# Optimization experiments

Measured on AMD Instinct MI355X. Metric: run time of the kernel, lower is better.

The kernel has to match this reference:

```python
import jax, jax.numpy as jnp
import numpy as np

ALPHA = 0.2      # LeakyReLU negative slope
NEG_BIG = -9e15  # mask value from the original module


def setup_inputs() -> dict:
    key = jax.random.key(0)
    kx, ka, kW, ka1, ka2, kb = jax.random.split(key, 6)
    B, N, F_in, F_out = 8, 2048, 256, 128
    x = jax.random.normal(kx, (B, N, F_in), dtype=jnp.float32)
    adj = (jax.random.uniform(ka, (B, N, N)) < 0.1).astype(jnp.float32)
    adj = adj.at[:, jnp.arange(N), jnp.arange(N)].set(1.0)
    # parameters (xavier-uniform-ish scaling)
    W = jax.random.normal(kW, (F_out, F_in), dtype=jnp.float32) * np.sqrt(2.0 / (F_in + F_out))
    a1 = jax.random.normal(ka1, (F_out,), dtype=jnp.float32) * np.sqrt(2.0 / (2 * F_out + 1))
    a2 = jax.random.normal(ka2, (F_out,), dtype=jnp.float32) * np.sqrt(2.0 / (2 * F_out + 1))
    a_b = jax.random.normal(kb, (1,), dtype=jnp.float32) * 0.01
    return {"x": x, "adj": adj, "W": W, "a1": a1, "a2": a2, "a_b": a_b}


def reference(x, adj, W, a1, a2, a_b):
    # h = W(input): [B, N, F_out]
    h = jnp.einsum('bnf,of->bno', x, W)
    # a([h_i, h_j]) == a1.h_i + a2.h_j + bias  (exact decomposition of the concat)
    s1 = h @ a1  # [B, N] contribution of row-repeated node i
    s2 = h @ a2  # [B, N] contribution of tiled node j
    e = jax.nn.leaky_relu(s1[:, :, None] + s2[:, None, :] + a_b[0], negative_slope=ALPHA)  # [B,N,N]
    att = jnp.where(adj > 0, e, NEG_BIG)
    att = jax.nn.softmax(att, axis=1)  # softmax over dim=1, as in the original
    # dropout is a no-op in eval mode
    att = att * adj
    h_prime = jnp.einsum('bij,bjo->bio', att, h)
    return jax.nn.elu(h_prime)  # concat=True -> ELU
```

## Files before the change

kernel.cpp:

```cpp
#include <hip/hip_runtime.h>
#include <stdint.h>

typedef unsigned int  uint32;
typedef unsigned long long u64;

#define L2E 1.44269504088896340736f

typedef float f32x4 __attribute__((ext_vector_type(4)));
typedef short bf16x8 __attribute__((ext_vector_type(8)));

__device__ __forceinline__ unsigned short f2bf(float f){
  uint32 u = __float_as_uint(f);
  u += 0x7fffu + ((u >> 16) & 1u);
  return (unsigned short)(u >> 16);
}


__global__ __launch_bounds__(256) void k_h(const float* __restrict__ x,
                                           const float* __restrict__ W,
                                           const float* __restrict__ a1,
                                           const float* __restrict__ a2,
                                           const float* __restrict__ ab,
                                           float* __restrict__ h,
                                           float* __restrict__ E1,
                                           float* __restrict__ E2p){
  __shared__ unsigned short xs[2][64][72];
  __shared__ unsigned short wsm[2][128][72];
  const int tid = threadIdx.x;
  const int wv = tid >> 6, lane = tid & 63;
  const int r = lane & 15, kg = lane >> 4;
  const int row0 = blockIdx.x * 64;

  f32x4 acc[8];
  #pragma unroll
  for (int of = 0; of < 8; ++of) acc[of] = (f32x4){0.f,0.f,0.f,0.f};

  for (int kc = 0; kc < 4; ++kc){
    if (kc) __syncthreads();
    #pragma unroll
    for (int it = 0; it < 4; ++it){
      int idx = tid + it * 256;
      int row = idx >> 4, f = (idx & 15) * 4;
      float4 v = *(const float4*)(x + (size_t)(row0 + row) * 256 + kc * 64 + f);
      ushort4 hi, lo;
      { unsigned short hh = f2bf(v.x); float rr = v.x - __uint_as_float(((uint32)hh)<<16); hi.x = hh; lo.x = f2bf(rr); }
      { unsigned short hh = f2bf(v.y); float rr = v.y - __uint_as_float(((uint32)hh)<<16); hi.y = hh; lo.y = f2bf(rr); }
      { unsigned short hh = f2bf(v.z); float rr = v.z - __uint_as_float(((uint32)hh)<<16); hi.z = hh; lo.z = f2bf(rr); }
      { unsigned short hh = f2bf(v.w); float rr = v.w - __uint_as_float(((uint32)hh)<<16); hi.w = hh; lo.w = f2bf(rr); }
      *(ushort4*)&xs[0][row][f] = hi;
      *(ushort4*)&xs[1][row][f] = lo;
    }
    #pragma unroll
    for (int it = 0; it < 8; ++it){
      int idx = tid + it * 256;
      int o = idx >> 4, f = (idx & 15) * 4;
      float4 v = *(const float4*)(W + (size_t)o * 256 + kc * 64 + f);
      ushort4 hi, lo;
      { unsigned short hh = f2bf(v.x); float rr = v.x - __uint_as_float(((uint32)hh)<<16); hi.x = hh; lo.x = f2bf(rr); }
      { unsigned short hh = f2bf(v.y); float rr = v.y - __uint_as_float(((uint32)hh)<<16); hi.y = hh; lo.y = f2bf(rr); }
      { unsigned short hh = f2bf(v.z); float rr = v.z - __uint_as_float(((uint32)hh)<<16); hi.z = hh; lo.z = f2bf(rr); }
      { unsigned short hh = f2bf(v.w); float rr = v.w - __uint_as_float(((uint32)hh)<<16); hi.w = hh; lo.w = f2bf(rr); }
      *(ushort4*)&wsm[0][o][f] = hi;
      *(ushort4*)&wsm[1][o][f] = lo;
    }
    __syncthreads();
    #pragma unroll
    for (int kk = 0; kk < 2; ++kk){
      bf16x8 ah = *(const bf16x8*)&xs[0][wv*16 + r][kk*32 + kg*8];
      bf16x8 al = *(const bf16x8*)&xs[1][wv*16 + r][kk*32 + kg*8];
      #pragma unroll
      for (int of = 0; of < 8; ++of){
        bf16x8 bh = *(const bf16x8*)&wsm[0][of*16 + r][kk*32 + kg*8];
        bf16x8 bl = *(const bf16x8*)&wsm[1][of*16 + r][kk*32 + kg*8];
        acc[of] = __builtin_amdgcn_mfma_f32_16x16x32_bf16(ah, bh, acc[of], 0, 0, 0);
        acc[of] = __builtin_amdgcn_mfma_f32_16x16x32_bf16(ah, bl, acc[of], 0, 0, 0);
        acc[of] = __builtin_amdgcn_mfma_f32_16x16x32_bf16(al, bh, acc[of], 0, 0, 0);
      }
    }
  }
  #pragma unroll
  for (int of = 0; of < 8; ++of)
    #pragma unroll
    for (int q = 0; q < 4; ++q)
      h[(size_t)(row0 + wv*16 + kg*4 + q) * 128 + of*16 + r] = acc[of][q];

  float p1[4] = {0,0,0,0}, p2[4] = {0,0,0,0};
  #pragma unroll
  for (int of = 0; of < 8; ++of){
    float w1 = a1[of*16 + r], w2 = a2[of*16 + r];
    #pragma unroll
    for (int q = 0; q < 4; ++q){
      p1[q] = fmaf(acc[of][q], w1, p1[q]);
      p2[q] = fmaf(acc[of][q], w2, p2[q]);
    }
  }
  #pragma unroll
  for (int off = 8; off; off >>= 1)
    #pragma unroll
    for (int q = 0; q < 4; ++q){
      p1[q] += __shfl_xor(p1[q], off);
      p2[q] += __shfl_xor(p2[q], off);
    }
  if (r == 0){
    float abv = ab[0];
    #pragma unroll
    for (int q = 0; q < 4; ++q){
      int row = row0 + wv*16 + kg*4 + q;
      E1[row] = p1[q] * L2E;
      int bb = row >> 11, j = row & 2047;
      int kp = (j & ~255) + (j & 3) * 64 + ((j & 255) >> 2);
      E2p[bb * 2048 + kp] = (p2[q] + abv) * L2E;
    }
  }
}

#define KDM_ROW(av, rr)                                                        \
  {                                                                            \
    const float e1 = e1p[rr];                                                  \
    float t0 = e1 + e2v[0]; t0 = fmaxf(t0, 0.2f * t0);                         \
    float t1 = e1 + e2v[1]; t1 = fmaxf(t1, 0.2f * t1);                         \
    float t2 = e1 + e2v[2]; t2 = fmaxf(t2, 0.2f * t2);                         \
    float t3 = e1 + e2v[3]; t3 = fmaxf(t3, 0.2f * t3);                         \
    ds0 = fmaf((av).x, __builtin_amdgcn_exp2f(t0), ds0);                       \
    ds1 = fmaf((av).y, __builtin_amdgcn_exp2f(t1), ds1);                       \
    ds2 = fmaf((av).z, __builtin_amdgcn_exp2f(t2), ds2);                       \
    ds3 = fmaf((av).w, __builtin_amdgcn_exp2f(t3), ds3);                       \
    u64 b0 = __ballot((av).x != 0.f);                                          \
    u64 b1 = __ballot((av).y != 0.f);                                          \
    u64 b2 = __ballot((av).z != 0.f);                                          \
    u64 b3 = __ballot((av).w != 0.f);                                          \
    if (lane == 0){                                                            \
      ulonglong2* dst = (ulonglong2*)(mp + (size_t)(rr) * 32);                 \
      dst[0] = (ulonglong2){b0, b1};                                           \
      dst[1] = (ulonglong2){b2, b3};                                           \
    }                                                                          \
  }

__global__ __launch_bounds__(256) void k_dm(const float* __restrict__ adj,
                                            const float* __restrict__ E1,
                                            const float* __restrict__ E2p,
                                            float* __restrict__ denomP,
                                            u64* __restrict__ mask){
  __shared__ float red[4][256];
  const int b = blockIdx.z, Q = blockIdx.x, ic = blockIdx.y;
  const int wv = threadIdx.x >> 6, lane = threadIdx.x & 63;
  const int Jbase = Q * 256;
  const int row0 = ic * 128 + wv * 32;

  const float* e1p = E1 + b * 2048 + row0;
  const float4* ap = (const float4*)(adj + (size_t)(b * 2048 + row0) * 2048 + Jbase) + lane;
  u64* mp = mask + (size_t)(b * 2048 + row0) * 32 + Q * 4;

  float e2v[4];
  #pragma unroll
  for (int p = 0; p < 4; ++p)
    e2v[p] = E2p[b * 2048 + Q * 256 + p * 64 + lane];

  float ds0 = 0.f, ds1 = 0.f, ds2 = 0.f, ds3 = 0.f;

  float4 avA[4], avB[4];
  #pragma unroll
  for (int u = 0; u < 4; ++u) avA[u] = ap[(size_t)u * 512];

  #pragma unroll
  for (int g = 0; g < 4; ++g){
    const int rA = g * 8;
    #pragma unroll
    for (int u = 0; u < 4; ++u) avB[u] = ap[(size_t)(rA + 4 + u) * 512];
    #pragma unroll
    for (int u = 0; u < 4; ++u) KDM_ROW(avA[u], rA + u)
    if (g < 3){
      #pragma unroll
      for (int u = 0; u < 4; ++u) avA[u] = ap[(size_t)(rA + 8 + u) * 512];
    }
    #pragma unroll
    for (int u = 0; u < 4; ++u) KDM_ROW(avB[u], rA + 4 + u)
  }

  *(float4*)&red[wv][lane * 4] = (float4){ds0, ds1, ds2, ds3};
  __syncthreads();
  const int t = threadIdx.x;
  denomP[ic * 16384 + b * 2048 + Jbase + t] = red[0][t] + red[1][t] + red[2][t] + red[3][t];
}

__global__ __launch_bounds__(256) void k_gt(const float* __restrict__ h,
                                            const float* __restrict__ denomP,
                                            unsigned short* __restrict__ gTp){
  __shared__ float hl[8464];
  __shared__ float rrec[256];
  const int b = blockIdx.z, Q = blockIdx.x, ot = blockIdx.y;
  const int o0 = ot * 32;
  const int tid = threadIdx.x;

  {
    float d = 0.f;
    #pragma unroll
    for (int ic = 0; ic < 16; ++ic)
      d += denomP[ic * 16384 + b * 2048 + Q * 256 + tid];
    rrec[tid] = 1.0f / d;
  }
  __syncthreads();

  #pragma unroll
  for (int it = 0; it < 8; ++it){
    int idx = tid + it * 256;
    int j = idx >> 3, f = idx & 7;
    float4 v = *(const float4*)(h + (size_t)(b * 2048 + Q * 256 + j) * 128 + o0 + f * 4);
    float rc = rrec[j];
    int base = j * 33 + (j >> 4) + f * 4;
    hl[base + 0] = v.x * rc;
    hl[base + 1] = v.y * rc;
    hl[base + 2] = v.z * rc;
    hl[base + 3] = v.w * rc;
  }
  __syncthreads();

  const int u  = tid & 127;
  const int fh = tid >> 7;
  const int lane = u >> 1;
  const int e0 = (u & 1) * 4;
  const int orow_r = lane & 15;
  const int kgrp = lane >> 4;
  #pragma unroll
  for (int it = 0; it < 8; ++it){
    int f  = it * 2 + fh;
    int kb = f >> 1, sl = f & 1;
    int orow = sl * 16 + orow_r;
    int klb = kb * 32 + kgrp * 8 + e0;
    ushort4 uu;
    { int kl = klb + 0; int jl = 4 * (kl & 63) + (kl >> 6); uu.x = f2bf(hl[jl * 33 + (jl >> 4) + orow]); }
    { int kl = klb + 1; int jl = 4 * (kl & 63) + (kl >> 6); uu.y = f2bf(hl[jl * 33 + (jl >> 4) + orow]); }
    { int kl = klb + 2; int jl = 4 * (kl & 63) + (kl >> 6); uu.z = f2bf(hl[jl * 33 + (jl >> 4) + orow]); }
    { int kl = klb + 3; int jl = 4 * (kl & 63) + (kl >> 6); uu.w = f2bf(hl[jl * 33 + (jl >> 4) + orow]); }
    size_t dst = ((size_t)((b * 64 + Q * 8 + kb) * 8 + (ot * 2 + sl))) * 512 + lane * 8 + e0;
    *(ushort4*)(gTp + dst) = uu;
  }
}

__global__ __launch_bounds__(256) void k_main(const float* __restrict__ E1,
                                              const float* __restrict__ E2p,
                                              const uint32* __restrict__ mask32,
                                              const unsigned short* __restrict__ gTp,
                                              float* __restrict__ out){
  __shared__ float cmb[4][32][129];
  const int b  = blockIdx.y;
  const int ib = blockIdx.x;
  const int wv = threadIdx.x >> 6, lane = threadIdx.x & 63;
  const int r  = lane & 15, kg = lane >> 4;
  const int gi0 = b * 2048 + ib * 32 + r;
  const float e1_0 = E1[gi0];
  const float e1_1 = E1[gi0 + 16];
  const uint32* m0 = mask32 + (size_t)gi0 * 64;
  const uint32* m1 = mask32 + (size_t)(gi0 + 16) * 64;

  f32x4 acc[2][8];
  #pragma unroll
  for (int si = 0; si < 2; ++si)
    #pragma unroll
    for (int so = 0; so < 8; ++so)
      acc[si][so] = (f32x4){0.f, 0.f, 0.f, 0.f};

  const int k0 = wv * 512, k1 = k0 + 512;
  for (int kk = k0; kk < k1; kk += 32){
    const int j0 = kk + kg * 8;
    const float4 eA = *(const float4*)(E2p + b * 2048 + j0);
    const float4 eB = *(const float4*)(E2p + b * 2048 + j0 + 4);
    const uint32 bits0 = (m0[kk >> 5] >> (kg * 8)) & 0xffu;
    const uint32 bits1 = (m1[kk >> 5] >> (kg * 8)) & 0xffu;
    float e2v[8] = {eA.x, eA.y, eA.z, eA.w, eB.x, eB.y, eB.z, eB.w};

    union { uint32 u[4]; bf16x8 v; } af0, af1;
    #pragma unroll
    for (int p = 0; p < 4; ++p){
      {
        float t0 = e1_0 + e2v[2*p];     t0 = fmaxf(t0, 0.2f * t0);
        float t1 = e1_0 + e2v[2*p+1];   t1 = fmaxf(t1, 0.2f * t1);
        float x0 = ((bits0 >> (2*p))   & 1u) ? __builtin_amdgcn_exp2f(t0) : 0.f;
        float x1 = ((bits0 >> (2*p+1)) & 1u) ? __builtin_amdgcn_exp2f(t1) : 0.f;
        uint32 u0 = __float_as_uint(x0); u0 = (u0 + 0x7fffu + ((u0 >> 16) & 1u)) >> 16;
        uint32 u1 = __float_as_uint(x1); u1 = (u1 + 0x7fffu + ((u1 >> 16) & 1u)) & 0xffff0000u;
        af0.u[p] = u0 | u1;
      }
      {
        float t0 = e1_1 + e2v[2*p];     t0 = fmaxf(t0, 0.2f * t0);
        float t1 = e1_1 + e2v[2*p+1];   t1 = fmaxf(t1, 0.2f * t1);
        float x0 = ((bits1 >> (2*p))   & 1u) ? __builtin_amdgcn_exp2f(t0) : 0.f;
        float x1 = ((bits1 >> (2*p+1)) & 1u) ? __builtin_amdgcn_exp2f(t1) : 0.f;
        uint32 u0 = __float_as_uint(x0); u0 = (u0 + 0x7fffu + ((u0 >> 16) & 1u)) >> 16;
        uint32 u1 = __float_as_uint(x1); u1 = (u1 + 0x7fffu + ((u1 >> 16) & 1u)) & 0xffff0000u;
        af1.u[p] = u0 | u1;
      }
    }
    const unsigned short* gk = gTp + ((size_t)(b * 64 + (kk >> 5)) * 8) * 512 + lane * 8;
    #pragma unroll
    for (int so = 0; so < 8; ++so){
      bf16x8 bfr = *(const bf16x8*)(gk + so * 512);
      acc[0][so] = __builtin_amdgcn_mfma_f32_16x16x32_bf16(af0.v, bfr, acc[0][so], 0, 0, 0);
      acc[1][so] = __builtin_amdgcn_mfma_f32_16x16x32_bf16(af1.v, bfr, acc[1][so], 0, 0, 0);
    }
  }

  #pragma unroll
  for (int si = 0; si < 2; ++si)
    #pragma unroll
    for (int so = 0; so < 8; ++so)
      #pragma unroll
      for (int q = 0; q < 4; ++q){
        int il = si * 16 + kg * 4 + q;
        int o  = so * 16 + r;
        cmb[wv][il][o] = acc[si][so][q];
      }
  __syncthreads();
  for (int e = threadIdx.x; e < 4096; e += 256){
    int i = e >> 7, o = e & 127;
    float v = cmb[0][i][o] + cmb[1][i][o] + cmb[2][i][o] + cmb[3][i][o];
    float res = v > 0.f ? v : (__builtin_amdgcn_exp2f(v * L2E) - 1.0f);
    out[(size_t)(b * 2048 + ib * 32 + i) * 128 + o] = res;
  }
}

extern "C" void kernel_launch(void* const* d_in, const int* in_sizes, int n_in,
                              void* d_out, int out_size, void* d_ws, size_t ws_size,
                              hipStream_t stream){
  const float* x   = (const float*)d_in[0];
  const float* adj = (const float*)d_in[1];
  const float* W   = (const float*)d_in[2];
  const float* a1  = (const float*)d_in[3];
  const float* a2  = (const float*)d_in[4];
  const float* ab  = (const float*)d_in[5];
  float* out = (float*)d_out;

  const size_t WS_NEEDED = 17956864;
  if (ws_size < WS_NEEDED) return;

  char* ws = (char*)d_ws;
  float* h      = (float*)(ws);
  float* E1     = (float*)(ws + 8388608);
  float* E2p    = (float*)(ws + 8454144);
  float* denomP = (float*)(ws + 8519680);
  u64*   mask   = (u64*)  (ws + 9568256);
  unsigned short* gTp = (unsigned short*)(ws + 13762560);

  k_h  <<<256, 256, 0, stream>>>(x, W, a1, a2, ab, h, E1, E2p);
  k_dm <<<dim3(8, 16, 8), 256, 0, stream>>>(adj, E1, E2p, denomP, mask);
  k_gt <<<dim3(8, 4, 8), 256, 0, stream>>>(h, denomP, gTp);
  k_main<<<dim3(64, 8), 256, 0, stream>>>(E1, E2p, (const uint32*)mask, gTp, out);
}
```

Measured before the change: 68.77 us.

## Restructure k_dm to process full rows per wave with coalesced mask stores

The adjacency-scan kernel now gives each block 32 full rows across all 2048 columns instead of a 256-column by 128-row tile. Each wave keeps all E2 values and 32 partial denominators in registers, and writes a row's mask with a single 32-lane coalesced store instead of lane-0 stores. The denominator partials grow from 16 to 64 slices, so a new k_red kernel sums them and computes reciprocals once rather than in every k_gt block. The gTp buffer is aliased onto denomP to shrink the workspace. This raises register pressure (8x4 partial sums plus two 8-wide float4 buffers), which may lower occupancy in a kernel bound by adjacency bandwidth, and it adds one extra kernel launch.

```diff
diff --git a/kernel.cpp b/kernel.cpp
--- a/kernel.cpp
+++ b/kernel.cpp
@@ -114,26 +114,30 @@
   }
 }
 
-#define KDM_ROW(av, rr)                                                        \
-  {                                                                            \
-    const float e1 = e1p[rr];                                                  \
-    float t0 = e1 + e2v[0]; t0 = fmaxf(t0, 0.2f * t0);                         \
-    float t1 = e1 + e2v[1]; t1 = fmaxf(t1, 0.2f * t1);                         \
-    float t2 = e1 + e2v[2]; t2 = fmaxf(t2, 0.2f * t2);                         \
-    float t3 = e1 + e2v[3]; t3 = fmaxf(t3, 0.2f * t3);                         \
-    ds0 = fmaf((av).x, __builtin_amdgcn_exp2f(t0), ds0);                       \
-    ds1 = fmaf((av).y, __builtin_amdgcn_exp2f(t1), ds1);                       \
-    ds2 = fmaf((av).z, __builtin_amdgcn_exp2f(t2), ds2);                       \
-    ds3 = fmaf((av).w, __builtin_amdgcn_exp2f(t3), ds3);                       \
-    u64 b0 = __ballot((av).x != 0.f);                                          \
-    u64 b1 = __ballot((av).y != 0.f);                                          \
-    u64 b2 = __ballot((av).z != 0.f);                                          \
-    u64 b3 = __ballot((av).w != 0.f);                                          \
-    if (lane == 0){                                                            \
-      ulonglong2* dst = (ulonglong2*)(mp + (size_t)(rr) * 32);                 \
-      dst[0] = (ulonglong2){b0, b1};                                           \
-      dst[1] = (ulonglong2){b2, b3};                                           \
-    }                                                                          \
+#define KDM_ROWC(av, rrr)                                                       \
+  {                                                                             \
+    const float e1 = e1r[rrr];                                                  \
+    u64 w = 0;                                                                  \
+    _Pragma("unroll")                                                           \
+    for (int c = 0; c < 8; ++c){                                                \
+      float t0 = e1 + e2v[c][0]; t0 = fmaxf(t0, 0.2f * t0);                     \
+      float t1 = e1 + e2v[c][1]; t1 = fmaxf(t1, 0.2f * t1);                     \
+      float t2 = e1 + e2v[c][2]; t2 = fmaxf(t2, 0.2f * t2);                     \
+      float t3 = e1 + e2v[c][3]; t3 = fmaxf(t3, 0.2f * t3);                     \
+      ds[c][0] = fmaf((av)[c].x, __builtin_amdgcn_exp2f(t0), ds[c][0]);         \
+      ds[c][1] = fmaf((av)[c].y, __builtin_amdgcn_exp2f(t1), ds[c][1]);         \
+      ds[c][2] = fmaf((av)[c].z, __builtin_amdgcn_exp2f(t2), ds[c][2]);         \
+      ds[c][3] = fmaf((av)[c].w, __builtin_amdgcn_exp2f(t3), ds[c][3]);         \
+      u64 b0 = __ballot((av)[c].x != 0.f);                                      \
+      u64 b1 = __ballot((av)[c].y != 0.f);                                      \
+      u64 b2 = __ballot((av)[c].z != 0.f);                                      \
+      u64 b3 = __ballot((av)[c].w != 0.f);                                      \
+      w = (lane == c * 4 + 0) ? b0 : w;                                         \
+      w = (lane == c * 4 + 1) ? b1 : w;                                         \
+      w = (lane == c * 4 + 2) ? b2 : w;                                         \
+      w = (lane == c * 4 + 3) ? b3 : w;                                         \
+    }                                                                           \
+    if (lane < 32) mp[(size_t)(rrr) * 32 + lane] = w;                           \
   }
 
 __global__ __launch_bounds__(256) void k_dm(const float* __restrict__ adj,
@@ -141,50 +145,72 @@
                                             const float* __restrict__ E2p,
                                             float* __restrict__ denomP,
                                             u64* __restrict__ mask){
-  __shared__ float red[4][256];
-  const int b = blockIdx.z, Q = blockIdx.x, ic = blockIdx.y;
+  __shared__ float red[4][2048];
+  const int bid = blockIdx.x;
+  const int b = bid >> 6, g = bid & 63;
   const int wv = threadIdx.x >> 6, lane = threadIdx.x & 63;
-  const int Jbase = Q * 256;
-  const int row0 = ic * 128 + wv * 32;
-
-  const float* e1p = E1 + b * 2048 + row0;
-  const float4* ap = (const float4*)(adj + (size_t)(b * 2048 + row0) * 2048 + Jbase) + lane;
-  u64* mp = mask + (size_t)(b * 2048 + row0) * 32 + Q * 4;
-
-  float e2v[4];
-  #pragma unroll
-  for (int p = 0; p < 4; ++p)
-    e2v[p] = E2p[b * 2048 + Q * 256 + p * 64 + lane];
-
-  float ds0 = 0.f, ds1 = 0.f, ds2 = 0.f, ds3 = 0.f;
-
-  float4 avA[4], avB[4];
-  #pragma unroll
-  for (int u = 0; u < 4; ++u) avA[u] = ap[(size_t)u * 512];
-
-  #pragma unroll
-  for (int g = 0; g < 4; ++g){
-    const int rA = g * 8;
-    #pragma unroll
-    for (int u = 0; u < 4; ++u) avB[u] = ap[(size_t)(rA + 4 + u) * 512];
-    #pragma unroll
-    for (int u = 0; u < 4; ++u) KDM_ROW(avA[u], rA + u)
-    if (g < 3){
+  const int row0 = b * 2048 + g * 32 + wv * 8;
+
+  float e2v[8][4];
+  #pragma unroll
+  for (int c = 0; c < 8; ++c)
+    #pragma unroll
+    for (int p = 0; p < 4; ++p)
+      e2v[c][p] = E2p[b * 2048 + c * 256 + p * 64 + lane];
+
+  float ds[8][4];
+  #pragma unroll
+  for (int c = 0; c < 8; ++c)
+    #pragma unroll
+    for (int p = 0; p < 4; ++p) ds[c][p] = 0.f;
+
+  const float4* ap = (const float4*)(adj + (size_t)row0 * 2048) + lane;
+  u64* mp = mask + (size_t)row0 * 32;
+
+  float4 e1a = *(const float4*)(E1 + row0);
+  float4 e1b = *(const float4*)(E1 + row0 + 4);
+  float e1r[8] = {e1a.x, e1a.y, e1a.z, e1a.w, e1b.x, e1b.y, e1b.z, e1b.w};
+
+  float4 avA[8], avB[8];
+  #pragma unroll
+  for (int c = 0; c < 8; ++c) avA[c] = ap[c * 64];
+
+  #pragma unroll
+  for (int rp = 0; rp < 4; ++rp){
+    const int r0 = rp * 2;
+    #pragma unroll
+    for (int c = 0; c < 8; ++c) avB[c] = ap[(size_t)(r0 + 1) * 512 + c * 64];
+    KDM_ROWC(avA, r0)
+    if (rp < 3){
       #pragma unroll
-      for (int u = 0; u < 4; ++u) avA[u] = ap[(size_t)(rA + 8 + u) * 512];
-    }
-    #pragma unroll
-    for (int u = 0; u < 4; ++u) KDM_ROW(avB[u], rA + 4 + u)
-  }
-
-  *(float4*)&red[wv][lane * 4] = (float4){ds0, ds1, ds2, ds3};
+      for (int c = 0; c < 8; ++c) avA[c] = ap[(size_t)(r0 + 2) * 512 + c * 64];
+    }
+    KDM_ROWC(avB, r0 + 1)
+  }
+
+  #pragma unroll
+  for (int c = 0; c < 8; ++c)
+    *(float4*)&red[wv][c * 256 + lane * 4] = (float4){ds[c][0], ds[c][1], ds[c][2], ds[c][3]};
   __syncthreads();
-  const int t = threadIdx.x;
-  denomP[ic * 16384 + b * 2048 + Jbase + t] = red[0][t] + red[1][t] + red[2][t] + red[3][t];
+  #pragma unroll
+  for (int it = 0; it < 8; ++it){
+    int j = it * 256 + threadIdx.x;
+    denomP[(size_t)g * 16384 + b * 2048 + j] = red[0][j] + red[1][j] + red[2][j] + red[3][j];
+  }
+}
+
+__global__ __launch_bounds__(256) void k_red(const float* __restrict__ denomP,
+                                             float* __restrict__ rinv){
+  const int n = blockIdx.x * 256 + threadIdx.x;
+  float s = 0.f;
+  #pragma unroll
+  for (int gg = 0; gg < 64; ++gg)
+    s += denomP[(size_t)gg * 16384 + n];
+  rinv[n] = 1.0f / s;
 }
 
 __global__ __launch_bounds__(256) void k_gt(const float* __restrict__ h,
-                                            const float* __restrict__ denomP,
+                                            const float* __restrict__ rinv,
                                             unsigned short* __restrict__ gTp){
   __shared__ float hl[8464];
   __shared__ float rrec[256];
@@ -192,13 +218,7 @@
   const int o0 = ot * 32;
   const int tid = threadIdx.x;
 
-  {
-    float d = 0.f;
-    #pragma unroll
-    for (int ic = 0; ic < 16; ++ic)
-      d += denomP[ic * 16384 + b * 2048 + Q * 256 + tid];
-    rrec[tid] = 1.0f / d;
-  }
+  rrec[tid] = rinv[b * 2048 + Q * 256 + tid];
   __syncthreads();
 
   #pragma unroll
@@ -330,19 +350,21 @@
   const float* ab  = (const float*)d_in[5];
   float* out = (float*)d_out;
 
-  const size_t WS_NEEDED = 17956864;
+  const size_t WS_NEEDED = 16973824;
   if (ws_size < WS_NEEDED) return;
 
   char* ws = (char*)d_ws;
   float* h      = (float*)(ws);
   float* E1     = (float*)(ws + 8388608);
   float* E2p    = (float*)(ws + 8454144);
-  float* denomP = (float*)(ws + 8519680);
-  u64*   mask   = (u64*)  (ws + 9568256);
-  unsigned short* gTp = (unsigned short*)(ws + 13762560);
+  float* rinv   = (float*)(ws + 8519680);
+  float* denomP = (float*)(ws + 8585216);
+  unsigned short* gTp = (unsigned short*)(ws + 8585216);
+  u64*   mask   = (u64*)  (ws + 12779520);
 
   k_h  <<<256, 256, 0, stream>>>(x, W, a1, a2, ab, h, E1, E2p);
-  k_dm <<<dim3(8, 16, 8), 256, 0, stream>>>(adj, E1, E2p, denomP, mask);
-  k_gt <<<dim3(8, 4, 8), 256, 0, stream>>>(h, denomP, gTp);
+  k_dm <<<512, 256, 0, stream>>>(adj, E1, E2p, denomP, mask);
+  k_red<<<64, 256, 0, stream>>>(denomP, rinv);
+  k_gt <<<dim3(8, 4, 8), 256, 0, stream>>>(h, rinv, gTp);
   k_main<<<dim3(64, 8), 256, 0, stream>>>(E1, E2p, (const uint32*)mask, gTp, out);
 }
```

After: 91.33 us. 1.33x slower.
